# Kernel optimization log

Measured on AMD Instinct MI355X. Metric: run time of the kernel, lower is better.

The kernel has to match this reference:

```python
import jax, jax.numpy as jnp
import numpy as np

VAR_NUM = [29, 2, 1, 6, 7, 59, 1, 24, 76, 711, 3, 9, 1]  # sums to 929
TEMP = 0.8
EPS = 1e-20


def setup_inputs() -> dict:
    key = jax.random.key(0)
    ks = jax.random.split(key, 8)
    B, D, H, O = 32768, 128, 1024, 929
    s = lambda n: 1.0 / np.sqrt(n)
    return {
        "x": jax.random.normal(ks[0], (B, D), jnp.float32),
        "W1": jax.random.uniform(ks[1], (D, H), jnp.float32, -s(D), s(D)),
        "b1": jax.random.uniform(ks[2], (H,), jnp.float32, -s(D), s(D)),
        "W2": jax.random.uniform(ks[3], (H, H), jnp.float32, -s(H), s(H)),
        "b2": jax.random.uniform(ks[4], (H,), jnp.float32, -s(H), s(H)),
        "W3": jax.random.uniform(ks[5], (H, O), jnp.float32, -s(H), s(H)),
        "b3": jax.random.uniform(ks[6], (O,), jnp.float32, -s(H), s(H)),
        "u": jax.random.uniform(ks[7], (B, O), jnp.float32),  # U(0,1) gumbel base noise
    }


def reference(x, W1, b1, W2, b2, W3, b3, u):
    h = jax.nn.elu(x @ W1 + b1)          # [B, H]
    h = jax.nn.sigmoid(h @ W2 + b2)      # [B, H]
    logits = h @ W3 + b3                 # [B, 929]
    g = -jnp.log(-jnp.log(u + EPS) + EPS)  # gumbel noise, [B, 929]
    outs = []
    off = 0
    for n in VAR_NUM:  # fixed 13 segments
        seg = logits[:, off:off + n]
        if n == 1:
            outs.append(seg)  # passthrough for continuous columns
        else:
            y = (seg + g[:, off:off + n]) / TEMP
            outs.append(jax.nn.softmax(y, axis=-1))
        off += n
    return jnp.concatenate(outs, axis=1)  # [B, 929]
```

## Files before the change

kernel.cpp:

```cpp
#include <hip/hip_runtime.h>
#include <hip/hip_bf16.h>
#include <stdint.h>

#define GEPS 1e-20f

typedef __bf16 bf16x8 __attribute__((ext_vector_type(8)));
typedef float  f32x4  __attribute__((ext_vector_type(4)));

typedef const __attribute__((address_space(1))) uint32_t* gptr32;
typedef __attribute__((address_space(3))) uint32_t* lptr32;

__device__ __forceinline__ void load_lds16(const void* g, void* l) {
    __builtin_amdgcn_global_load_lds((gptr32)g, (lptr32)l, 16, 0, 0);
}

__device__ __forceinline__ uint16_t f2bf(float v) {
    __hip_bfloat16 b = __float2bfloat16(v);
    return *(uint16_t*)&b;
}
__device__ __forceinline__ float bf2f(uint16_t b) {
    uint32_t u = (uint32_t)b << 16;
    return __builtin_bit_cast(float, u);
}

#define LN2   0.69314718056f
#define LOG2E 1.44269504089f
__device__ __forceinline__ float fast_log(float x) { return __builtin_amdgcn_logf(x) * LN2; }
__device__ __forceinline__ float fast_exp(float x) { return __builtin_amdgcn_exp2f(x * LOG2E); }
__device__ __forceinline__ float fast_exp2(float x) { return __builtin_amdgcn_exp2f(x); }

__device__ __forceinline__ void store_val(uint16_t* C, size_t idx, float v) { C[idx] = f2bf(v); }
__device__ __forceinline__ void store_val(float* C, size_t idx, float v)    { C[idx] = v; }

__global__ void cast_bf16(const float* __restrict__ in, uint16_t* __restrict__ out, int n) {
    int i = (blockIdx.x * blockDim.x + threadIdx.x) * 4;
    if (i < n) {
        float4 v = *(const float4*)(in + i);
        ushort4 o;
        o.x = f2bf(v.x); o.y = f2bf(v.y); o.z = f2bf(v.z); o.w = f2bf(v.w);
        *(ushort4*)(out + i) = o;
    }
}

__global__ void transpose_cast(const float* __restrict__ W, uint16_t* __restrict__ Wt,
                               int K, int N, int Npad) {
    __shared__ float tile[64][65];
    const int k0 = blockIdx.y * 64, n0 = blockIdx.x * 64;
    const int tx = threadIdx.x & 63, ty = threadIdx.x >> 6;
    for (int r = ty; r < 64; r += 4) {
        int n = n0 + tx;
        tile[r][tx] = (n < N) ? W[(size_t)(k0 + r) * N + n] : 0.f;
    }
    __syncthreads();
    for (int r = ty; r < 64; r += 4) {
        Wt[(size_t)(n0 + r) * K + k0 + tx] = f2bf(tile[tx][r]);
    }
}

template<int ACT, typename OutT, bool SNG>
__global__ __launch_bounds__(256)
void gemm_bt(const uint16_t* __restrict__ A, const uint16_t* __restrict__ Bt,
             const float* __restrict__ bias, OutT* __restrict__ C,
             float* __restrict__ sngl,
             int K, int Nout, int ldc) {
    __shared__ __align__(16) uint16_t As[128 * 32];
    __shared__ __align__(16) uint16_t Bs[128 * 32];

    const int t    = threadIdx.x;
    const int wave = t >> 6, lane = t & 63;

    const int nbx = gridDim.x;
    const int bid = blockIdx.y * nbx + blockIdx.x;
    const int xcd = bid & 7;
    const int s   = bid >> 3;
    const int nidx = s % nbx;
    const int midx = xcd * (gridDim.y >> 3) + s / nbx;

    const int m0 = midx * 128, n0 = nidx * 128;
    const int wm = (wave >> 1) * 64, wn = (wave & 1) * 64;
    const int quad = lane >> 4;
    const int qk   = quad * 8;
    const int r15  = lane & 15;

    f32x4 acc[4][4] = {};

    const uint16_t* Ag = A  + (size_t)m0 * K;
    const uint16_t* Bg = Bt + (size_t)n0 * K;

    for (int k0 = 0; k0 < K; k0 += 32) {
        __syncthreads();
        #pragma unroll
        for (int rd = 0; rd < 2; ++rd) {
            int c = t + rd * 256;
            int row = c >> 2, kc = (c & 3) * 8;
            load_lds16(Ag + (size_t)row * K + k0 + kc, &As[c * 8]);
            load_lds16(Bg + (size_t)row * K + k0 + kc, &Bs[c * 8]);
        }
        __syncthreads();

        bf16x8 a[4], b[4];
        #pragma unroll
        for (int i = 0; i < 4; ++i)
            a[i] = *(const bf16x8*)&As[(wm + i * 16 + r15) * 32 + qk];
        #pragma unroll
        for (int i = 0; i < 4; ++i)
            b[i] = *(const bf16x8*)&Bs[(wn + i * 16 + r15) * 32 + qk];

        #pragma unroll
        for (int mi = 0; mi < 4; ++mi)
            #pragma unroll
            for (int ni = 0; ni < 4; ++ni)
                acc[mi][ni] = __builtin_amdgcn_mfma_f32_16x16x32_bf16(
                    a[mi], b[ni], acc[mi][ni], 0, 0, 0);
    }

    #pragma unroll
    for (int ni = 0; ni < 4; ++ni) {
        int col = n0 + wn + ni * 16 + r15;
        if (col < Nout) {
            float bv = bias[col];
            bool is_sng = SNG && (col == 31 || col == 104 || col == 928);
            #pragma unroll
            for (int mi = 0; mi < 4; ++mi) {
                #pragma unroll
                for (int r = 0; r < 4; ++r) {
                    int row = m0 + wm + mi * 16 + quad * 4 + r;
                    float v = acc[mi][ni][r] + bv;
                    if (ACT == 1) v = (v > 0.f) ? v : (fast_exp(v) - 1.f);
                    else if (ACT == 2) v = 1.f / (1.f + fast_exp(-v));
                    store_val(C, (size_t)row * ldc + col, v);
                    if constexpr (SNG) {
                        if (is_sng) sngl[(size_t)row * 929 + col] = v;
                    }
                }
            }
        }
    }
}

__global__ __launch_bounds__(256)
void gumbel_epilogue(const uint16_t* __restrict__ lg, float* __restrict__ out,
                     const float* __restrict__ u, int B) {
    constexpr int NSEG = 13;
    constexpr int SEGN[NSEG] = {29, 2, 1, 6, 7, 59, 1, 24, 76, 711, 3, 9, 1};
    __shared__ float buf[4][712];

    const int wave = threadIdx.x >> 6, lane = threadIdx.x & 63;
    const int row = blockIdx.x * 4 + wave;
    if (row >= B) return;

    const uint16_t* rlg = lg + (size_t)row * 929;
    float* rout = out + (size_t)row * 929;
    const float* ru = u + (size_t)row * 929;
    float* wb = buf[wave];

    int off = 0;
    #pragma unroll
    for (int s = 0; s < NSEG; ++s) {
        const int n = SEGN[s];
        if (n > 1) {
            float lmax = -3.4e38f;
            for (int j = lane; j < n; j += 64) {
                float g = -fast_log(-fast_log(ru[off + j] + GEPS) + GEPS);
                float y = (bf2f(rlg[off + j]) + g) * 1.25f;
                wb[j] = y;
                lmax = fmaxf(lmax, y);
            }
            #pragma unroll
            for (int o = 32; o > 0; o >>= 1) lmax = fmaxf(lmax, __shfl_xor(lmax, o, 64));
            float lsum = 0.f;
            for (int j = lane; j < n; j += 64) {
                float e = fast_exp2((wb[j] - lmax) * LOG2E);
                wb[j] = e;
                lsum += e;
            }
            #pragma unroll
            for (int o = 32; o > 0; o >>= 1) lsum += __shfl_xor(lsum, o, 64);
            float inv = 1.f / lsum;
            for (int j = lane; j < n; j += 64) rout[off + j] = wb[j] * inv;
        }
        off += n;
    }
}

extern "C" void kernel_launch(void* const* d_in, const int* in_sizes, int n_in,
                              void* d_out, int out_size, void* d_ws, size_t ws_size,
                              hipStream_t stream) {
    const float* x  = (const float*)d_in[0];
    const float* W1 = (const float*)d_in[1];
    const float* b1 = (const float*)d_in[2];
    const float* W2 = (const float*)d_in[3];
    const float* b2 = (const float*)d_in[4];
    const float* W3 = (const float*)d_in[5];
    const float* b3 = (const float*)d_in[6];
    const float* u  = (const float*)d_in[7];
    float* out = (float*)d_out;

    const int B = 32768, D = 128, H = 1024, O = 929, OP = 1024;

    char* ws = (char*)d_ws;
    uint16_t* xb  = (uint16_t*)ws; ws += (size_t)B * D * 2;
    uint16_t* w1t = (uint16_t*)ws; ws += (size_t)H * D * 2;
    uint16_t* w2t = (uint16_t*)ws; ws += (size_t)H * H * 2;
    uint16_t* w3t = (uint16_t*)ws; ws += (size_t)OP * H * 2;
    uint16_t* h1  = (uint16_t*)ws; ws += (size_t)B * H * 2;
    uint16_t* h2  = (uint16_t*)ws; ws += (size_t)B * H * 2;
    uint16_t* lg  = h1;

    cast_bf16<<<(B * D / 4 + 255) / 256, 256, 0, stream>>>(x, xb, B * D);
    transpose_cast<<<dim3(H / 64, D / 64), 256, 0, stream>>>(W1, w1t, D, H, H);
    transpose_cast<<<dim3(H / 64, H / 64), 256, 0, stream>>>(W2, w2t, H, H, H);
    transpose_cast<<<dim3(OP / 64, H / 64), 256, 0, stream>>>(W3, w3t, H, O, OP);

    gemm_bt<1, uint16_t, false><<<dim3(H / 128, B / 128), 256, 0, stream>>>(
        xb, w1t, b1, h1, nullptr, D, H, H);
    gemm_bt<2, uint16_t, false><<<dim3(H / 128, B / 128), 256, 0, stream>>>(
        h1, w2t, b2, h2, nullptr, H, H, H);
    gemm_bt<0, uint16_t, true><<<dim3(OP / 128, B / 128), 256, 0, stream>>>(
        h2, w3t, b3, lg, out, H, O, O);

    gumbel_epilogue<<<B / 4, 256, 0, stream>>>(lg, out, u, B);
}
```

Measured before the change: 541.9 us.

## Restructure gumbel softmax epilogue with register-resident segments and half-wave small segments

Rewrites the gumbel-softmax epilogue so each wave processes two rows. Small segments are handled by 32-lane half-waves using narrow shuffle reductions, and wide segments keep their values in registers instead of an LDS buffer. The scale and log2 constants are folded into single FMAs, and divides are replaced with hardware reciprocal, including in the sigmoid GEMM epilogue. The goals are less LDS traffic, fewer idle lanes on the small segments, and less ALU work. In exchange, the fixed segment offsets are hard-coded and the approximate reciprocal may shift precision slightly.

```diff
diff --git a/kernel.cpp b/kernel.cpp
--- a/kernel.cpp
+++ b/kernel.cpp
@@ -28,6 +28,7 @@
 __device__ __forceinline__ float fast_log(float x) { return __builtin_amdgcn_logf(x) * LN2; }
 __device__ __forceinline__ float fast_exp(float x) { return __builtin_amdgcn_exp2f(x * LOG2E); }
 __device__ __forceinline__ float fast_exp2(float x) { return __builtin_amdgcn_exp2f(x); }
+__device__ __forceinline__ float fast_rcp(float x)  { return __builtin_amdgcn_rcpf(x); }
 
 __device__ __forceinline__ void store_val(uint16_t* C, size_t idx, float v) { C[idx] = f2bf(v); }
 __device__ __forceinline__ void store_val(float* C, size_t idx, float v)    { C[idx] = v; }
@@ -127,7 +128,7 @@
                     int row = m0 + wm + mi * 16 + quad * 4 + r;
                     float v = acc[mi][ni][r] + bv;
                     if (ACT == 1) v = (v > 0.f) ? v : (fast_exp(v) - 1.f);
-                    else if (ACT == 2) v = 1.f / (1.f + fast_exp(-v));
+                    else if (ACT == 2) v = fast_rcp(1.f + fast_exp(-v));
                     store_val(C, (size_t)row * ldc + col, v);
                     if constexpr (SNG) {
                         if (is_sng) sngl[(size_t)row * 929 + col] = v;
@@ -138,49 +139,99 @@
     }
 }
 
+#define NEG_BIG (-1e30f)
+#define Y2_LG   1.8033688011f
+
+__device__ __forceinline__ float y2_col(const uint16_t* __restrict__ rlg,
+                                        const float* __restrict__ ru, int c) {
+    float l2u   = __builtin_amdgcn_logf(ru[c] + GEPS);
+    float inner = fmaf(-LN2, l2u, GEPS);
+    float l2i   = __builtin_amdgcn_logf(inner);
+    return fmaf(Y2_LG, bf2f(rlg[c]), -1.25f * l2i);
+}
+
+template<int N, int OFF>
+__device__ __forceinline__ void seg_small(const uint16_t* __restrict__ rlg,
+                                          const float* __restrict__ ru,
+                                          float* __restrict__ rout, int l32) {
+    static_assert(N <= 32, "seg_small needs N<=32");
+    constexpr int GS = (N <= 2) ? 2 : (N <= 4) ? 4 : (N <= 8) ? 8 : (N <= 16) ? 16 : 32;
+    const bool act = l32 < N;
+    const int  c   = OFF + l32;
+    float y = act ? y2_col(rlg, ru, c) : NEG_BIG;
+    float m = y;
+    #pragma unroll
+    for (int o = 1; o < GS; o <<= 1) m = fmaxf(m, __shfl_xor(m, o, 64));
+    float e = act ? fast_exp2(y - m) : 0.f;
+    float s = e;
+    #pragma unroll
+    for (int o = 1; o < GS; o <<= 1) s += __shfl_xor(s, o, 64);
+    if (act) rout[c] = e * fast_rcp(s);
+}
+
+template<int N, int OFF>
+__device__ __forceinline__ void seg_wide(const uint16_t* __restrict__ rlg,
+                                         const float* __restrict__ ru,
+                                         float* __restrict__ rout, int lane) {
+    constexpr int IT = (N + 63) / 64;
+    float y[IT];
+    float m = NEG_BIG;
+    #pragma unroll
+    for (int i = 0; i < IT; ++i) {
+        const int j = i * 64 + lane;
+        y[i] = (j < N) ? y2_col(rlg, ru, OFF + j) : NEG_BIG;
+        m = fmaxf(m, y[i]);
+    }
+    #pragma unroll
+    for (int o = 1; o < 64; o <<= 1) m = fmaxf(m, __shfl_xor(m, o, 64));
+    float s = 0.f;
+    #pragma unroll
+    for (int i = 0; i < IT; ++i) {
+        float e = fast_exp2(y[i] - m);
+        y[i] = e;
+        s += e;
+    }
+    #pragma unroll
+    for (int o = 1; o < 64; o <<= 1) s += __shfl_xor(s, o, 64);
+    const float inv = fast_rcp(s);
+    #pragma unroll
+    for (int i = 0; i < IT; ++i) {
+        const int j = i * 64 + lane;
+        if (j < N) rout[OFF + j] = y[i] * inv;
+    }
+}
+
 __global__ __launch_bounds__(256)
 void gumbel_epilogue(const uint16_t* __restrict__ lg, float* __restrict__ out,
                      const float* __restrict__ u, int B) {
-    constexpr int NSEG = 13;
-    constexpr int SEGN[NSEG] = {29, 2, 1, 6, 7, 59, 1, 24, 76, 711, 3, 9, 1};
-    __shared__ float buf[4][712];
-
     const int wave = threadIdx.x >> 6, lane = threadIdx.x & 63;
-    const int row = blockIdx.x * 4 + wave;
-    if (row >= B) return;
-
-    const uint16_t* rlg = lg + (size_t)row * 929;
-    float* rout = out + (size_t)row * 929;
-    const float* ru = u + (size_t)row * 929;
-    float* wb = buf[wave];
-
-    int off = 0;
-    #pragma unroll
-    for (int s = 0; s < NSEG; ++s) {
-        const int n = SEGN[s];
-        if (n > 1) {
-            float lmax = -3.4e38f;
-            for (int j = lane; j < n; j += 64) {
-                float g = -fast_log(-fast_log(ru[off + j] + GEPS) + GEPS);
-                float y = (bf2f(rlg[off + j]) + g) * 1.25f;
-                wb[j] = y;
-                lmax = fmaxf(lmax, y);
-            }
-            #pragma unroll
-            for (int o = 32; o > 0; o >>= 1) lmax = fmaxf(lmax, __shfl_xor(lmax, o, 64));
-            float lsum = 0.f;
-            for (int j = lane; j < n; j += 64) {
-                float e = fast_exp2((wb[j] - lmax) * LOG2E);
-                wb[j] = e;
-                lsum += e;
-            }
-            #pragma unroll
-            for (int o = 32; o > 0; o >>= 1) lsum += __shfl_xor(lsum, o, 64);
-            float inv = 1.f / lsum;
-            for (int j = lane; j < n; j += 64) rout[off + j] = wb[j] * inv;
-        }
-        off += n;
-    }
+    const int l32  = lane & 31, half = lane >> 5;
+    const int rowA = blockIdx.x * 8 + wave * 2;
+    if (rowA >= B) return;
+
+    const size_t baseA = (size_t)rowA * 929;
+    const size_t baseB = baseA + 929;
+    const size_t baseH = half ? baseB : baseA;
+
+    const uint16_t* lgH = lg  + baseH;
+    const float*    uH  = u   + baseH;
+    float*          oH  = out + baseH;
+    seg_small<29,   0>(lgH, uH, oH, l32);
+    seg_small< 2,  29>(lgH, uH, oH, l32);
+    seg_small< 6,  32>(lgH, uH, oH, l32);
+    seg_small< 7,  38>(lgH, uH, oH, l32);
+    seg_small<24, 105>(lgH, uH, oH, l32);
+    seg_small< 3, 916>(lgH, uH, oH, l32);
+    seg_small< 9, 919>(lgH, uH, oH, l32);
+
+    const uint16_t* lgA = lg + baseA; const float* uA = u + baseA; float* oA = out + baseA;
+    const uint16_t* lgB = lg + baseB; const float* uB = u + baseB; float* oB = out + baseB;
+    seg_wide< 59,  45>(lgA, uA, oA, lane);
+    seg_wide< 59,  45>(lgB, uB, oB, lane);
+    seg_wide< 76, 129>(lgA, uA, oA, lane);
+    seg_wide< 76, 129>(lgB, uB, oB, lane);
+    seg_wide<711, 205>(lgA, uA, oA, lane);
+    seg_wide<711, 205>(lgB, uB, oB, lane);
 }
 
 extern "C" void kernel_launch(void* const* d_in, const int* in_sizes, int n_in,
@@ -219,5 +270,5 @@
     gemm_bt<0, uint16_t, true><<<dim3(OP / 128, B / 128), 256, 0, stream>>>(
         h2, w3t, b3, lg, out, H, O, O);
 
-    gumbel_epilogue<<<B / 4, 256, 0, stream>>>(lg, out, u, B);
-}
+    gumbel_epilogue<<<B / 8, 256, 0, stream>>>(lg, out, u, B);
+}
```

Result: faster. 507.1 us (-6.4%).
